# Performance work log

Hardware: AMD Instinct MI355X
Metric: run time of the kernel (lower is better)

The kernel has to match this reference:

```python
import jax, jax.numpy as jnp
import numpy as np

N_NODES = 50000
N_EDGES = 800000
NFEAT, NHID, NCLASS = 512, 128, 40


def _glorot(key, fan_in, fan_out):
    # mimics the usual GCN uniform init: U(-1/sqrt(fan_out), 1/sqrt(fan_out))
    stdv = 1.0 / np.sqrt(fan_out)
    return jax.random.uniform(key, (fan_in, fan_out), jnp.float32, -stdv, stdv)


def setup_inputs() -> dict:
    key = jax.random.key(0)
    ks = jax.random.split(key, 8)
    x = jax.random.normal(ks[0], (N_NODES, NFEAT), jnp.float32)
    edge_src = jax.random.randint(ks[1], (N_EDGES,), 0, N_NODES)
    edge_dst = jax.random.randint(ks[2], (N_EDGES,), 0, N_NODES)
    edge_weight = jax.random.uniform(ks[3], (N_EDGES,), jnp.float32)
    W1 = _glorot(ks[4], NFEAT, NHID)
    b1 = jnp.zeros((NHID,), jnp.float32)
    W2 = _glorot(ks[5], NHID, NCLASS)
    b2 = jnp.zeros((NCLASS,), jnp.float32)
    return {"x": x, "edge_src": edge_src, "edge_dst": edge_dst,
            "edge_weight": edge_weight, "W1": W1, "b1": b1, "W2": W2, "b2": b2}


def _gcn_layer(x, W, b, edge_src, edge_dst, edge_weight):
    # support = x @ W ; out = spmm(adj, support) + b
    support = x @ W                                   # [N, F_out]
    msgs = support[edge_src] * edge_weight[:, None]   # [E, F_out]
    agg = jax.ops.segment_sum(msgs, edge_dst, num_segments=N_NODES)
    return agg + b


def reference(x, edge_src, edge_dst, edge_weight, W1, b1, W2, b2):
    h = _gcn_layer(x, W1, b1, edge_src, edge_dst, edge_weight)
    h = jax.nn.relu(h)
    # F.dropout(training=False) -> identity in eval mode
    out = _gcn_layer(h, W2, b2, edge_src, edge_dst, edge_weight)
    return out
```

## Files before the change

kernel.cpp:

```cpp
#include <hip/hip_runtime.h>


#define F0 512
#define F1 128
#define F2 40
#define F2P 48

typedef short bf16x8 __attribute__((ext_vector_type(8)));
typedef float f32x4 __attribute__((ext_vector_type(4)));

static __device__ __forceinline__ unsigned short f2b(float f){
    union { float f; unsigned int u; } x; x.f = f;
    unsigned int u = x.u;
    unsigned int r = (u + 0x7fffu + ((u >> 16) & 1u)) >> 16;
    return (unsigned short)r;
}
static __device__ __forceinline__ unsigned short f2b_fast(float f){
    return (unsigned short)((__float_as_uint(f) + 0x8000u) >> 16);
}
static __device__ __forceinline__ unsigned int pack2(float a, float b){
    unsigned int ua = __float_as_uint(a) + 0x8000u;
    unsigned int ub = __float_as_uint(b) + 0x8000u;
    return __builtin_amdgcn_perm(ub, ua, 0x07060302u);
}
static __device__ __forceinline__ bf16x8 pack8(float4 v0, float4 v1){
    union { bf16x8 v; unsigned int d[4]; } r;
    r.d[0] = pack2(v0.x, v0.y);
    r.d[1] = pack2(v0.z, v0.w);
    r.d[2] = pack2(v1.x, v1.y);
    r.d[3] = pack2(v1.z, v1.w);
    return r.v;
}
static __device__ __forceinline__ float b2f(unsigned short h){
    union { unsigned int u; float f; } x; x.u = ((unsigned int)h) << 16; return x.f;
}

__global__ void hist_kernel(const int* __restrict__ dst, int* __restrict__ cnt, int E){
    int e = blockIdx.x*256 + threadIdx.x;
    if (e < E) atomicAdd(&cnt[dst[e]], 1);
}

__global__ void scan1_kernel(const int* __restrict__ cnt, int* __restrict__ offs,
                             int* __restrict__ bsum, int n){
    __shared__ int sd[256];
    int tid = threadIdx.x;
    int base = blockIdx.x*1024 + tid*4;
    int c0 = (base+0<n)?cnt[base+0]:0;
    int c1 = (base+1<n)?cnt[base+1]:0;
    int c2 = (base+2<n)?cnt[base+2]:0;
    int c3 = (base+3<n)?cnt[base+3]:0;
    int v1=c0, v2=c0+c1, v3=c0+c1+c2;
    int s = c0+c1+c2+c3;
    sd[tid]=s; __syncthreads();
    for (int off=1; off<256; off<<=1){
        int t = (tid>=off)? sd[tid-off] : 0;
        __syncthreads();
        sd[tid] += t;
        __syncthreads();
    }
    int excl = sd[tid] - s;
    if (base+0<n) offs[base+0]=excl;
    if (base+1<n) offs[base+1]=excl+v1;
    if (base+2<n) offs[base+2]=excl+v2;
    if (base+3<n) offs[base+3]=excl+v3;
    if (tid==255) bsum[blockIdx.x]=sd[255];
}

__global__ void scan3_kernel(int* __restrict__ offs, int* __restrict__ cur,
                             const int* __restrict__ bsum, int n, int E, int nb){
    __shared__ int sexcl;
    int tid = threadIdx.x;
    if (tid < 64){
        int v = (tid < nb) ? bsum[tid] : 0;
        int orig = v;
        #pragma unroll
        for (int off=1; off<64; off<<=1){
            int t = __shfl_up(v, off);
            if (tid >= off) v += t;
        }
        int g = blockIdx.x >> 2;
        if (tid == g) sexcl = v - orig;
    }
    __syncthreads();
    int i = blockIdx.x*256 + tid;
    if (i<n){ int o = offs[i] + sexcl; offs[i]=o; cur[i]=o; }
    if (i==0) offs[n]=E;
}

__global__ void scatter_kernel(const int* __restrict__ src, const int* __restrict__ dst,
                               const float* __restrict__ w, int* __restrict__ cur,
                               int2* __restrict__ edges, int E){
    int e = blockIdx.x*256+threadIdx.x;
    if (e<E){
        int d = dst[e];
        int pos = atomicAdd(&cur[d],1);
        int2 rec; rec.x = src[e]; rec.y = __float_as_int(w[e]);
        edges[pos] = rec;
    }
}

__global__ void prep_w(const float* __restrict__ W1, const float* __restrict__ W2,
                       unsigned short* __restrict__ W1t, unsigned short* __restrict__ W2t){
    int idx = blockIdx.x*256 + threadIdx.x;
    if (idx < F0*F1){
        int k = idx >> 7, n = idx & 127;
        W1t[(size_t)n*F0 + k] = f2b(W1[idx]);
    } else {
        int j = idx - F0*F1;
        if (j < F2P*F1){
            int n = j >> 7, k = j & 127;
            float v = (n < F2) ? W2[(size_t)k*F2 + n] : 0.f;
            W2t[j] = f2b(v);
        }
    }
}

__global__ __launch_bounds__(256) void gemm1_mfma(const float* __restrict__ X,
                                                  const unsigned short* __restrict__ W1t,
                                                  unsigned short* __restrict__ S1, int M){
    __shared__ unsigned short sB[128][72];
    int tid = threadIdx.x;
    int wave = tid >> 6, lane = tid & 63;
    int quad = lane >> 4, l16 = lane & 15;
    int row0 = blockIdx.x * 64;
    int myrow = row0 + wave*16 + l16;
    int arow = min(myrow, M-1);
    const float* xrow = X + (size_t)arow * F0;

    int sn = tid >> 1, shalf = tid & 1;
    const unsigned short* bsrc = W1t + (size_t)sn*F0 + shalf*32;
    unsigned short* bdst = &sB[sn][shalf*32];

    f32x4 acc[8];
    #pragma unroll
    for (int c=0;c<8;c++) acc[c] = (f32x4){0.f,0.f,0.f,0.f};

    float4 a0 = *(const float4*)(xrow + quad*8);
    float4 a1 = *(const float4*)(xrow + quad*8 + 4);
    float4 a2 = *(const float4*)(xrow + 32 + quad*8);
    float4 a3 = *(const float4*)(xrow + 32 + quad*8 + 4);
    {
        float4 b0 = *(const float4*)(bsrc+ 0), b1 = *(const float4*)(bsrc+ 8);
        float4 b2 = *(const float4*)(bsrc+16), b3 = *(const float4*)(bsrc+24);
        *(float4*)(bdst+ 0)=b0; *(float4*)(bdst+ 8)=b1;
        *(float4*)(bdst+16)=b2; *(float4*)(bdst+24)=b3;
    }
    __syncthreads();

    for (int k0 = 0; k0 < F0; k0 += 64){
        bool more = (k0 + 64) < F0;
        float4 na0, na1, na2, na3, nb0, nb1, nb2, nb3;
        if (more){
            const float* nx = xrow + k0 + 64;
            na0 = *(const float4*)(nx + quad*8);
            na1 = *(const float4*)(nx + quad*8 + 4);
            na2 = *(const float4*)(nx + 32 + quad*8);
            na3 = *(const float4*)(nx + 32 + quad*8 + 4);
            const unsigned short* p = bsrc + k0 + 64;
            nb0 = *(const float4*)(p+ 0); nb1 = *(const float4*)(p+ 8);
            nb2 = *(const float4*)(p+16); nb3 = *(const float4*)(p+24);
        }
        bf16x8 af0 = pack8(a0, a1);
        bf16x8 af1 = pack8(a2, a3);
        #pragma unroll
        for (int c=0;c<8;c++){
            bf16x8 b0 = *(bf16x8*)&sB[c*16 + l16][quad*8];
            bf16x8 b1 = *(bf16x8*)&sB[c*16 + l16][32 + quad*8];
            acc[c] = __builtin_amdgcn_mfma_f32_16x16x32_bf16(af0, b0, acc[c], 0, 0, 0);
            acc[c] = __builtin_amdgcn_mfma_f32_16x16x32_bf16(af1, b1, acc[c], 0, 0, 0);
        }
        if (more){
            __syncthreads();
            *(float4*)(bdst+ 0)=nb0; *(float4*)(bdst+ 8)=nb1;
            *(float4*)(bdst+16)=nb2; *(float4*)(bdst+24)=nb3;
            __syncthreads();
            a0 = na0; a1 = na1; a2 = na2; a3 = na3;
        }
    }
    #pragma unroll
    for (int c=0;c<8;c++){
        #pragma unroll
        for (int r=0;r<4;r++){
            int grow = row0 + wave*16 + quad*4 + r;
            if (grow < M) S1[(size_t)grow*F1 + c*16 + l16] = f2b_fast(acc[c][r]);
        }
    }
}

__global__ void agg1_kernel(const ushort2* __restrict__ S1, const int* __restrict__ offs,
                            const int2* __restrict__ edges,
                            const float* __restrict__ b1, ushort2* __restrict__ H, int n){
    int node = blockIdx.x*4 + (threadIdx.x >> 6);
    int lane = threadIdx.x & 63;
    if (node >= n) return;
    int e0 = offs[node], e1 = offs[node+1];
    double ax = 0.0, ay = 0.0;
    int e = e0;
    for (; e+8 <= e1; e += 8){
        int2 p0=edges[e],   p1=edges[e+1], p2=edges[e+2], p3=edges[e+3];
        int2 p4=edges[e+4], p5=edges[e+5], p6=edges[e+6], p7=edges[e+7];
        ushort2 v0 = S1[(size_t)p0.x*64 + lane];
        ushort2 v1 = S1[(size_t)p1.x*64 + lane];
        ushort2 v2 = S1[(size_t)p2.x*64 + lane];
        ushort2 v3 = S1[(size_t)p3.x*64 + lane];
        ushort2 v4 = S1[(size_t)p4.x*64 + lane];
        ushort2 v5 = S1[(size_t)p5.x*64 + lane];
        ushort2 v6 = S1[(size_t)p6.x*64 + lane];
        ushort2 v7 = S1[(size_t)p7.x*64 + lane];
        double w0=__int_as_float(p0.y), w1=__int_as_float(p1.y);
        double w2=__int_as_float(p2.y), w3=__int_as_float(p3.y);
        double w4=__int_as_float(p4.y), w5=__int_as_float(p5.y);
        double w6=__int_as_float(p6.y), w7=__int_as_float(p7.y);
        ax += w0*b2f(v0.x)+w1*b2f(v1.x)+w2*b2f(v2.x)+w3*b2f(v3.x)
            + w4*b2f(v4.x)+w5*b2f(v5.x)+w6*b2f(v6.x)+w7*b2f(v7.x);
        ay += w0*b2f(v0.y)+w1*b2f(v1.y)+w2*b2f(v2.y)+w3*b2f(v3.y)
            + w4*b2f(v4.y)+w5*b2f(v5.y)+w6*b2f(v6.y)+w7*b2f(v7.y);
    }
    for (; e < e1; e++){
        int2 p = edges[e];
        double w = __int_as_float(p.y);
        ushort2 v = S1[(size_t)p.x*64 + lane];
        ax += w*b2f(v.x); ay += w*b2f(v.y);
    }
    float2 bb = ((const float2*)b1)[lane];
    float vx = (float)(ax + (double)bb.x);
    float vy = (float)(ay + (double)bb.y);
    ushort2 o;
    o.x = f2b_fast(vx > 0.f ? vx : 0.f);
    o.y = f2b_fast(vy > 0.f ? vy : 0.f);
    H[(size_t)node*64 + lane] = o;
}

__global__ __launch_bounds__(256) void gemm2_mfma(const unsigned short* __restrict__ H,
                                                  const unsigned short* __restrict__ W2t,
                                                  unsigned short* __restrict__ S2, int M){
    __shared__ unsigned short sB[48][136];
    int tid = threadIdx.x;
    int wave = tid >> 6, lane = tid & 63;
    int quad = lane >> 4, l16 = lane & 15;
    for (int i = tid; i < 48*16; i += 256){
        int nn = i >> 4, p = i & 15;
        *(float4*)&sB[nn][p*8] = *(const float4*)&W2t[(size_t)nn*F1 + p*8];
    }
    int row0 = blockIdx.x * 64;
    int myrow = row0 + wave*16 + l16;
    int arow = min(myrow, M-1);
    const unsigned short* hrow = H + (size_t)arow * F1;
    bf16x8 a[4];
    #pragma unroll
    for (int ks=0; ks<4; ks++) a[ks] = *(const bf16x8*)(hrow + ks*32 + quad*8);
    __syncthreads();
    f32x4 acc[3];
    #pragma unroll
    for (int c=0;c<3;c++) acc[c] = (f32x4){0.f,0.f,0.f,0.f};
    #pragma unroll
    for (int ks=0; ks<4; ks++){
        #pragma unroll
        for (int c=0;c<3;c++){
            bf16x8 b = *(bf16x8*)&sB[c*16 + l16][ks*32 + quad*8];
            acc[c] = __builtin_amdgcn_mfma_f32_16x16x32_bf16(a[ks], b, acc[c], 0, 0, 0);
        }
    }
    #pragma unroll
    for (int c=0;c<3;c++){
        #pragma unroll
        for (int r=0;r<4;r++){
            int grow = row0 + wave*16 + quad*4 + r;
            if (grow < M) S2[(size_t)grow*F2P + c*16 + l16] = f2b_fast(acc[c][r]);
        }
    }
}

__global__ void agg2_kernel(const unsigned short* __restrict__ S2, const int* __restrict__ offs,
                            const int2* __restrict__ edges,
                            const float* __restrict__ b2, float* __restrict__ out, int n){
    int node = blockIdx.x*4 + (threadIdx.x >> 6);
    int lane = threadIdx.x & 63;
    if (node >= n) return;
    int e0 = offs[node], e1 = offs[node+1];
    bool act = lane < 20;
    double ax = 0.0, ay = 0.0;
    int e = e0;
    for (; e+4 <= e1; e += 4){
        int2 p0=edges[e], p1=edges[e+1], p2=edges[e+2], p3=edges[e+3];
        if (act){
            ushort2 v0 = *(const ushort2*)&S2[(size_t)p0.x*F2P + lane*2];
            ushort2 v1 = *(const ushort2*)&S2[(size_t)p1.x*F2P + lane*2];
            ushort2 v2 = *(const ushort2*)&S2[(size_t)p2.x*F2P + lane*2];
            ushort2 v3 = *(const ushort2*)&S2[(size_t)p3.x*F2P + lane*2];
            double w0=__int_as_float(p0.y), w1=__int_as_float(p1.y);
            double w2=__int_as_float(p2.y), w3=__int_as_float(p3.y);
            ax += w0*b2f(v0.x)+w1*b2f(v1.x)+w2*b2f(v2.x)+w3*b2f(v3.x);
            ay += w0*b2f(v0.y)+w1*b2f(v1.y)+w2*b2f(v2.y)+w3*b2f(v3.y);
        }
    }
    for (; e < e1; e++){
        int2 p = edges[e];
        if (act){
            double w = __int_as_float(p.y);
            ushort2 v = *(const ushort2*)&S2[(size_t)p.x*F2P + lane*2];
            ax += w*b2f(v.x); ay += w*b2f(v.y);
        }
    }
    if (act){
        float2 bb = ((const float2*)b2)[lane];
        float2 o;
        o.x = (float)(ax + (double)bb.x);
        o.y = (float)(ay + (double)bb.y);
        *(float2*)&out[(size_t)node*F2 + lane*2] = o;
    }
}

extern "C" void kernel_launch(void* const* d_in, const int* in_sizes, int n_in,
                              void* d_out, int out_size, void* d_ws, size_t ws_size,
                              hipStream_t stream){
    const float* x    = (const float*)d_in[0];
    const int*   esrc = (const int*)d_in[1];
    const int*   edst = (const int*)d_in[2];
    const float* ew   = (const float*)d_in[3];
    const float* W1   = (const float*)d_in[4];
    const float* b1   = (const float*)d_in[5];
    const float* W2   = (const float*)d_in[6];
    const float* b2   = (const float*)d_in[7];
    float* out = (float*)d_out;
    int N = in_sizes[0] / F0;
    int E = in_sizes[1];

    char* ws = (char*)d_ws;
    size_t off = 0;
    auto alloc = [&](size_t bytes)->void*{
        void* p = ws + off; off += (bytes + 255) & ~(size_t)255; return p;
    };
    unsigned short* S1 = (unsigned short*)alloc(sizeof(unsigned short)*(size_t)N*F1);
    unsigned short* H  = (unsigned short*)alloc(sizeof(unsigned short)*(size_t)N*F1);
    unsigned short* S2 = (unsigned short*)alloc(sizeof(unsigned short)*(size_t)N*F2P);
    unsigned short* W1t = (unsigned short*)alloc(sizeof(unsigned short)*F1*F0);
    unsigned short* W2t = (unsigned short*)alloc(sizeof(unsigned short)*F2P*F1);
    int*   offs  = (int*)alloc(sizeof(int)*(size_t)(N+1));
    int*   cur   = (int*)alloc(sizeof(int)*(size_t)N);
    int2*  edges = (int2*)alloc(sizeof(int2)*(size_t)E);
    int*   bsum  = (int*)alloc(sizeof(int)*64);

    hipMemsetAsync(cur, 0, sizeof(int)*(size_t)N, stream);
    hist_kernel<<<(E+255)/256,256,0,stream>>>(edst, cur, E);
    int nb = (N+1023)/1024;
    scan1_kernel<<<nb,256,0,stream>>>(cur, offs, bsum, N);
    scan3_kernel<<<(N+255)/256,256,0,stream>>>(offs, cur, bsum, N, E, nb);
    scatter_kernel<<<(E+255)/256,256,0,stream>>>(esrc, edst, ew, cur, edges, E);

    prep_w<<<(F0*F1 + F2P*F1 + 255)/256,256,0,stream>>>(W1, W2, W1t, W2t);

    gemm1_mfma<<<(N+63)/64,256,0,stream>>>(x, W1t, S1, N);
    agg1_kernel<<<(N+3)/4,256,0,stream>>>((const ushort2*)S1, offs, edges, b1, (ushort2*)H, N);
    gemm2_mfma<<<(N+63)/64,256,0,stream>>>(H, W2t, S2, N);
    agg2_kernel<<<(N+3)/4,256,0,stream>>>(S2, offs, edges, b2, out, N);
}
```

Baseline: 355.6 us.

## Pack edge records into 32 bits and split aggregation waves across edges

The CSR edge record shrinks from an int2 to one 32-bit word: the source index sits in the high 16 bits and the weight is stored as fp16 in the low 16 bits. This halves edge-list traffic. agg1 now splits each wave into two 32-lane halves that handle alternate edges with 4-wide feature loads, then combines the halves with a shuffle. agg2 uses four 16-lane groups so more lanes do useful work in the gather. The packing assumes fewer than 65536 nodes and loses weight precision by going to fp16.

```diff
diff --git a/kernel.cpp b/kernel.cpp
--- a/kernel.cpp
+++ b/kernel.cpp
@@ -33,6 +33,12 @@
 }
 static __device__ __forceinline__ float b2f(unsigned short h){
     union { unsigned int u; float f; } x; x.u = ((unsigned int)h) << 16; return x.f;
+}
+static __device__ __forceinline__ unsigned short f2h(float f){
+    union { _Float16 h; unsigned short u; } x; x.h = (_Float16)f; return x.u;
+}
+static __device__ __forceinline__ float h2f(unsigned short u){
+    union { unsigned short u; _Float16 h; } x; x.u = u; return (float)x.h;
 }
 
 __global__ void hist_kernel(const int* __restrict__ dst, int* __restrict__ cnt, int E){
@@ -89,13 +95,12 @@
 
 __global__ void scatter_kernel(const int* __restrict__ src, const int* __restrict__ dst,
                                const float* __restrict__ w, int* __restrict__ cur,
-                               int2* __restrict__ edges, int E){
+                               unsigned int* __restrict__ edges, int E){
     int e = blockIdx.x*256+threadIdx.x;
     if (e<E){
         int d = dst[e];
         int pos = atomicAdd(&cur[d],1);
-        int2 rec; rec.x = src[e]; rec.y = __float_as_int(w[e]);
-        edges[pos] = rec;
+        edges[pos] = ((unsigned int)src[e] << 16) | (unsigned int)f2h(w[e]);
     }
 }
 
@@ -187,48 +192,58 @@
     }
 }
 
-__global__ void agg1_kernel(const ushort2* __restrict__ S1, const int* __restrict__ offs,
-                            const int2* __restrict__ edges,
-                            const float* __restrict__ b1, ushort2* __restrict__ H, int n){
+__global__ void agg1_kernel(const unsigned short* __restrict__ S1, const int* __restrict__ offs,
+                            const unsigned int* __restrict__ edges,
+                            const float* __restrict__ b1, unsigned short* __restrict__ H, int n){
     int node = blockIdx.x*4 + (threadIdx.x >> 6);
     int lane = threadIdx.x & 63;
     if (node >= n) return;
+    int half = lane >> 5, fl = lane & 31;
     int e0 = offs[node], e1 = offs[node+1];
-    double ax = 0.0, ay = 0.0;
+    double a0=0.0, a1=0.0, a2=0.0, a3=0.0;
     int e = e0;
     for (; e+8 <= e1; e += 8){
-        int2 p0=edges[e],   p1=edges[e+1], p2=edges[e+2], p3=edges[e+3];
-        int2 p4=edges[e+4], p5=edges[e+5], p6=edges[e+6], p7=edges[e+7];
-        ushort2 v0 = S1[(size_t)p0.x*64 + lane];
-        ushort2 v1 = S1[(size_t)p1.x*64 + lane];
-        ushort2 v2 = S1[(size_t)p2.x*64 + lane];
-        ushort2 v3 = S1[(size_t)p3.x*64 + lane];
-        ushort2 v4 = S1[(size_t)p4.x*64 + lane];
-        ushort2 v5 = S1[(size_t)p5.x*64 + lane];
-        ushort2 v6 = S1[(size_t)p6.x*64 + lane];
-        ushort2 v7 = S1[(size_t)p7.x*64 + lane];
-        double w0=__int_as_float(p0.y), w1=__int_as_float(p1.y);
-        double w2=__int_as_float(p2.y), w3=__int_as_float(p3.y);
-        double w4=__int_as_float(p4.y), w5=__int_as_float(p5.y);
-        double w6=__int_as_float(p6.y), w7=__int_as_float(p7.y);
-        ax += w0*b2f(v0.x)+w1*b2f(v1.x)+w2*b2f(v2.x)+w3*b2f(v3.x)
-            + w4*b2f(v4.x)+w5*b2f(v5.x)+w6*b2f(v6.x)+w7*b2f(v7.x);
-        ay += w0*b2f(v0.y)+w1*b2f(v1.y)+w2*b2f(v2.y)+w3*b2f(v3.y)
-            + w4*b2f(v4.y)+w5*b2f(v5.y)+w6*b2f(v6.y)+w7*b2f(v7.y);
-    }
-    for (; e < e1; e++){
-        int2 p = edges[e];
-        double w = __int_as_float(p.y);
-        ushort2 v = S1[(size_t)p.x*64 + lane];
-        ax += w*b2f(v.x); ay += w*b2f(v.y);
-    }
-    float2 bb = ((const float2*)b1)[lane];
-    float vx = (float)(ax + (double)bb.x);
-    float vy = (float)(ay + (double)bb.y);
-    ushort2 o;
-    o.x = f2b_fast(vx > 0.f ? vx : 0.f);
-    o.y = f2b_fast(vy > 0.f ? vy : 0.f);
-    H[(size_t)node*64 + lane] = o;
+        unsigned int rA = edges[e   + half];
+        unsigned int rB = edges[e+2 + half];
+        unsigned int rC = edges[e+4 + half];
+        unsigned int rD = edges[e+6 + half];
+        ushort4 vA = *(const ushort4*)&S1[((size_t)(rA>>16))*F1 + fl*4];
+        ushort4 vB = *(const ushort4*)&S1[((size_t)(rB>>16))*F1 + fl*4];
+        ushort4 vC = *(const ushort4*)&S1[((size_t)(rC>>16))*F1 + fl*4];
+        ushort4 vD = *(const ushort4*)&S1[((size_t)(rD>>16))*F1 + fl*4];
+        double wA = h2f((unsigned short)rA), wB = h2f((unsigned short)rB);
+        double wC = h2f((unsigned short)rC), wD = h2f((unsigned short)rD);
+        a0 += wA*b2f(vA.x) + wB*b2f(vB.x) + wC*b2f(vC.x) + wD*b2f(vD.x);
+        a1 += wA*b2f(vA.y) + wB*b2f(vB.y) + wC*b2f(vC.y) + wD*b2f(vD.y);
+        a2 += wA*b2f(vA.z) + wB*b2f(vB.z) + wC*b2f(vC.z) + wD*b2f(vD.z);
+        a3 += wA*b2f(vA.w) + wB*b2f(vB.w) + wC*b2f(vC.w) + wD*b2f(vD.w);
+    }
+    for (; e < e1; e += 2){
+        int ee = e + half;
+        if (ee < e1){
+            unsigned int r = edges[ee];
+            ushort4 v = *(const ushort4*)&S1[((size_t)(r>>16))*F1 + fl*4];
+            double w = h2f((unsigned short)r);
+            a0 += w*b2f(v.x); a1 += w*b2f(v.y); a2 += w*b2f(v.z); a3 += w*b2f(v.w);
+        }
+    }
+    a0 += __shfl_down(a0, 32);
+    a1 += __shfl_down(a1, 32);
+    a2 += __shfl_down(a2, 32);
+    a3 += __shfl_down(a3, 32);
+    if (lane < 32){
+        float4 bb = *(const float4*)&b1[fl*4];
+        float o0 = (float)(a0 + (double)bb.x);
+        float o1 = (float)(a1 + (double)bb.y);
+        float o2 = (float)(a2 + (double)bb.z);
+        float o3 = (float)(a3 + (double)bb.w);
+        o0 = o0>0.f?o0:0.f; o1 = o1>0.f?o1:0.f;
+        o2 = o2>0.f?o2:0.f; o3 = o3>0.f?o3:0.f;
+        union { ushort4 v; unsigned int d[2]; } o;
+        o.d[0] = pack2(o0, o1);
+        o.d[1] = pack2(o2, o3);
+        *(ushort4*)&H[(size_t)node*F1 + fl*4] = o.v;
+    }
 }
 
 __global__ __launch_bounds__(256) void gemm2_mfma(const unsigned short* __restrict__ H,
@@ -272,42 +287,36 @@
 }
 
 __global__ void agg2_kernel(const unsigned short* __restrict__ S2, const int* __restrict__ offs,
-                            const int2* __restrict__ edges,
+                            const unsigned int* __restrict__ edges,
                             const float* __restrict__ b2, float* __restrict__ out, int n){
     int node = blockIdx.x*4 + (threadIdx.x >> 6);
     int lane = threadIdx.x & 63;
     if (node >= n) return;
+    int grp = lane >> 4, gl = lane & 15;
+    bool act = gl < 10;
     int e0 = offs[node], e1 = offs[node+1];
-    bool act = lane < 20;
-    double ax = 0.0, ay = 0.0;
-    int e = e0;
-    for (; e+4 <= e1; e += 4){
-        int2 p0=edges[e], p1=edges[e+1], p2=edges[e+2], p3=edges[e+3];
-        if (act){
-            ushort2 v0 = *(const ushort2*)&S2[(size_t)p0.x*F2P + lane*2];
-            ushort2 v1 = *(const ushort2*)&S2[(size_t)p1.x*F2P + lane*2];
-            ushort2 v2 = *(const ushort2*)&S2[(size_t)p2.x*F2P + lane*2];
-            ushort2 v3 = *(const ushort2*)&S2[(size_t)p3.x*F2P + lane*2];
-            double w0=__int_as_float(p0.y), w1=__int_as_float(p1.y);
-            double w2=__int_as_float(p2.y), w3=__int_as_float(p3.y);
-            ax += w0*b2f(v0.x)+w1*b2f(v1.x)+w2*b2f(v2.x)+w3*b2f(v3.x);
-            ay += w0*b2f(v0.y)+w1*b2f(v1.y)+w2*b2f(v2.y)+w3*b2f(v3.y);
-        }
-    }
-    for (; e < e1; e++){
-        int2 p = edges[e];
-        if (act){
-            double w = __int_as_float(p.y);
-            ushort2 v = *(const ushort2*)&S2[(size_t)p.x*F2P + lane*2];
-            ax += w*b2f(v.x); ay += w*b2f(v.y);
-        }
-    }
-    if (act){
-        float2 bb = ((const float2*)b2)[lane];
-        float2 o;
-        o.x = (float)(ax + (double)bb.x);
-        o.y = (float)(ay + (double)bb.y);
-        *(float2*)&out[(size_t)node*F2 + lane*2] = o;
+    double a0=0.0, a1=0.0, a2=0.0, a3=0.0;
+    for (int e = e0; e < e1; e += 4){
+        int ee = e + grp;
+        if (ee < e1 && act){
+            unsigned int r = edges[ee];
+            ushort4 v = *(const ushort4*)&S2[((size_t)(r>>16))*F2P + gl*4];
+            double w = h2f((unsigned short)r);
+            a0 += w*b2f(v.x); a1 += w*b2f(v.y); a2 += w*b2f(v.z); a3 += w*b2f(v.w);
+        }
+    }
+    a0 += __shfl_down(a0, 32); a0 += __shfl_down(a0, 16);
+    a1 += __shfl_down(a1, 32); a1 += __shfl_down(a1, 16);
+    a2 += __shfl_down(a2, 32); a2 += __shfl_down(a2, 16);
+    a3 += __shfl_down(a3, 32); a3 += __shfl_down(a3, 16);
+    if (lane < 10){
+        float4 bb = *(const float4*)&b2[lane*4];
+        float4 o;
+        o.x = (float)(a0 + (double)bb.x);
+        o.y = (float)(a1 + (double)bb.y);
+        o.z = (float)(a2 + (double)bb.z);
+        o.w = (float)(a3 + (double)bb.w);
+        *(float4*)&out[(size_t)node*F2 + lane*4] = o;
     }
 }
 
@@ -338,7 +347,7 @@
     unsigned short* W2t = (unsigned short*)alloc(sizeof(unsigned short)*F2P*F1);
     int*   offs  = (int*)alloc(sizeof(int)*(size_t)(N+1));
     int*   cur   = (int*)alloc(sizeof(int)*(size_t)N);
-    int2*  edges = (int2*)alloc(sizeof(int2)*(size_t)E);
+    unsigned int* edges = (unsigned int*)alloc(sizeof(unsigned int)*(size_t)E);
     int*   bsum  = (int*)alloc(sizeof(int)*64);
 
     hipMemsetAsync(cur, 0, sizeof(int)*(size_t)N, stream);
@@ -351,7 +360,7 @@
     prep_w<<<(F0*F1 + F2P*F1 + 255)/256,256,0,stream>>>(W1, W2, W1t, W2t);
 
     gemm1_mfma<<<(N+63)/64,256,0,stream>>>(x, W1t, S1, N);
-    agg1_kernel<<<(N+3)/4,256,0,stream>>>((const ushort2*)S1, offs, edges, b1, (ushort2*)H, N);
+    agg1_kernel<<<(N+3)/4,256,0,stream>>>(S1, offs, edges, b1, H, N);
     gemm2_mfma<<<(N+63)/64,256,0,stream>>>(H, W2t, S2, N);
     agg2_kernel<<<(N+3)/4,256,0,stream>>>(S2, offs, edges, b2, out, N);
 }
```

Measured after the change: 344.6 us. -3.1%, faster.
